# Optimization experiments

Hardware: AMD Instinct MI355X
Metric: run time of the kernel (lower is better)

## Reference

```python
import jax, jax.numpy as jnp
import numpy as np
from jax import lax

# config (mirrors Mamba3Config)
D_MODEL = 1024
D_STATE = 64
EXPAND = 2
HEADDIM = 64
D_INNER = EXPAND * D_MODEL            # 2048
NH = D_INNER // HEADDIM               # 32
N_ANG = D_STATE // 2                  # 32 rope angle channels
A_FLOOR = 1e-4
BATCH, SEQ = 2, 512
D_IN_PROJ = D_INNER + D_INNER + D_STATE + D_STATE + NH + NH + NH + N_ANG


def _layernorm(x, g, b, eps=1e-5):
    m = x.mean(-1, keepdims=True)
    v = ((x - m) ** 2).mean(-1, keepdims=True)
    return (x - m) / jnp.sqrt(v + eps) * g + b


def _rope_pairs(v, ang):
    # v: (..., S) even S; ang: (..., S//2). Rotate interleaved pairs.
    ve, vo = v[..., 0::2], v[..., 1::2]
    c, s = jnp.cos(ang), jnp.sin(ang)
    re = ve * c - vo * s
    ro = ve * s + vo * c
    return jnp.stack([re, ro], axis=-1).reshape(v.shape)


def setup_inputs() -> dict:
    key = jax.random.key(0)
    ks = jax.random.split(key, 9)
    u = jax.random.normal(ks[0], (BATCH, SEQ, D_MODEL), jnp.float32)
    W_in = jax.random.normal(ks[1], (D_MODEL, D_IN_PROJ), jnp.float32) * 0.02
    W_out = jax.random.normal(ks[2], (D_INNER, D_MODEL), jnp.float32) * 0.02
    dt_bias = jax.random.normal(ks[3], (NH,), jnp.float32) * 0.1
    D_param = jnp.ones((NH,), jnp.float32)
    Bn_g = 1.0 + 0.1 * jax.random.normal(ks[4], (D_STATE,), jnp.float32)
    Bn_b = 0.1 * jax.random.normal(ks[5], (D_STATE,), jnp.float32)
    Cn_g = 1.0 + 0.1 * jax.random.normal(ks[6], (D_STATE,), jnp.float32)
    Cn_b = 0.1 * jax.random.normal(ks[7], (D_STATE,), jnp.float32)
    return {"u": u, "W_in": W_in, "W_out": W_out, "dt_bias": dt_bias,
            "D_param": D_param, "Bn_g": Bn_g, "Bn_b": Bn_b,
            "Cn_g": Cn_g, "Cn_b": Cn_b}


def reference(u, W_in, W_out, dt_bias, D_param, Bn_g, Bn_b, Cn_g, Cn_b):
    B_, L, _ = u.shape
    proj = u @ W_in  # (B,L,D_IN_PROJ)
    idx = np.cumsum([D_INNER, D_INNER, D_STATE, D_STATE, NH, NH, NH])
    z, x, Bp, Cp, dd_dt, dd_A, trap_raw, angles = jnp.split(proj, idx, axis=-1)
    x4 = x.reshape(B_, L, NH, HEADDIM)
    z4 = z.reshape(B_, L, NH, HEADDIM)

    Bp = _layernorm(Bp, Bn_g, Bn_b)
    Cp = _layernorm(Cp, Cn_g, Cn_b)

    DT = jax.nn.softplus(dd_dt + dt_bias)            # (B,L,NH)
    DT_mean = DT.mean(axis=-1, keepdims=True)        # (B,L,1)
    phase = jnp.cumsum(angles * DT_mean, axis=1)     # (B,L,N_ANG)
    Bp_rot = _rope_pairs(Bp, phase)                  # (B,L,dS)
    Cp_rot = _rope_pairs(Cp, phase)

    A = jnp.minimum(-jax.nn.softplus(dd_A), -A_FLOOR)
    decay = jnp.exp(A * DT)                          # (B,L,NH)
    trap = jax.nn.sigmoid(trap_raw)                  # (B,L,NH)

    # Bx_all: (B,L,NH,hD,dS)  (B/C shared across heads -> broadcast in einsum)
    Bx = jnp.einsum('blhp,bln->blhpn', x4, Bp_rot)
    Bx_prev = jnp.pad(Bx[:, :-1], ((0, 0), (1, 0), (0, 0), (0, 0), (0, 0)))
    te = trap[..., None, None]
    inp = (te * Bx + (1.0 - te) * Bx_prev) * DT[..., None, None]

    # sequential selective scan over L
    decay_t = jnp.moveaxis(decay, 1, 0)   # (L,B,NH)
    inp_t = jnp.moveaxis(inp, 1, 0)       # (L,B,NH,hD,dS)
    C_t = jnp.moveaxis(Cp_rot, 1, 0)      # (L,B,dS)

    def step(h, xs):
        d, ip, c = xs
        h = d[:, :, None, None] * h + ip
        y = jnp.einsum('bhpn,bn->bhp', h, c)
        return h, y

    h0 = jnp.zeros((B_, NH, HEADDIM, D_STATE), u.dtype)
    _, ys = lax.scan(step, h0, (decay_t, inp_t, C_t))
    y = jnp.moveaxis(ys, 0, 1)                        # (B,L,NH,hD)
    y = (y + D_param[None, None, :, None] * x4) * jax.nn.silu(z4)
    out = y.reshape(B_, L, D_INNER) @ W_out
    return out
```

## Files before the change

### kernel.cpp

```cpp
#include <hip/hip_runtime.h>
#include <hip/hip_bf16.h>
#include <math.h>

#define B_   2
#define L_   512
#define DM   1024
#define DIP  4352
#define DPROJ 4224
#define DI   2048
#define NH_  32
#define HD   64
#define DS   64
#define NA   32
#define BL   (B_ * L_)
#define CHK  32
#define NCH  16
#define PB   (BL * 128)

#define OFF_Z    0
#define OFF_X    2048
#define OFF_BP   4096
#define OFF_CP   4160

typedef short bf16x8s __attribute__((ext_vector_type(8)));
typedef float f32x4 __attribute__((ext_vector_type(4)));

#define GL2LDS(gp, lp) __builtin_amdgcn_global_load_lds( \
    (const __attribute__((address_space(1))) unsigned int*)(const void*)(gp), \
    (__attribute__((address_space(3))) unsigned int*)(void*)(lp), 16, 0, 0)

__device__ __forceinline__ float softplusf(float x) {
    return x > 0.f ? x + log1pf(expf(-x)) : log1pf(expf(x));
}
__device__ __forceinline__ float sigmoidf_(float x) {
    return 1.f / (1.f + expf(-x));
}
__device__ __forceinline__ float wave_sum(float v) {
#pragma unroll
    for (int off = 32; off; off >>= 1) v += __shfl_xor(v, off);
    return v;
}
__device__ __forceinline__ ushort f2bf(float f) {
    uint u = __float_as_uint(f);
    return (ushort)((u + 0x7fffu + ((u >> 16) & 1u)) >> 16);
}
__device__ __forceinline__ float bf2f(ushort v) {
    return __uint_as_float((uint)v << 16);
}
__device__ __forceinline__ float4 ld_bf4(const ushort* p) {
    uint2 v = *(const uint2*)p;
    float4 r;
    r.x = __uint_as_float(v.x << 16);
    r.y = __uint_as_float(v.x & 0xffff0000u);
    r.z = __uint_as_float(v.y << 16);
    r.w = __uint_as_float(v.y & 0xffff0000u);
    return r;
}
__device__ __forceinline__ void st_bf4(ushort* p, float4 f) {
    uint2 v;
    v.x = (uint)f2bf(f.x) | ((uint)f2bf(f.y) << 16);
    v.y = (uint)f2bf(f.z) | ((uint)f2bf(f.w) << 16);
    *(uint2*)p = v;
}

__global__ __launch_bounds__(256) void prep_all(const float* __restrict__ u,
                                                const float* __restrict__ W_in,
                                                const float* __restrict__ W_out,
                                                ushort* __restrict__ ubf,
                                                ushort* __restrict__ WinT,
                                                ushort* __restrict__ WoutT,
                                                float* __restrict__ pbuf) {
    __shared__ float smem[2560];
    const int blk = blockIdx.x;
    const int tid = threadIdx.x;

    if (blk < 1600) {
        ushort (*t2)[72] = (ushort(*)[72])smem;
        const float* in;
        ushort* outp;
        int R, C, c0, r0;
        if (blk < 1088) {
            in = W_in; outp = WinT; R = DM; C = DIP;
            c0 = (blk % 68) * 64; r0 = (blk / 68) * 64;
        } else {
            const int bi = blk - 1088;
            in = W_out; outp = WoutT; R = DI; C = DM;
            c0 = (bi % 16) * 64; r0 = (bi / 16) * 64;
        }
        const int cq = tid & 15;
        const int rrb = tid >> 4;
#pragma unroll
        for (int j = 0; j < 4; ++j) {
            const int rr = j * 16 + rrb;
            float4 v = *(const float4*)&in[(size_t)(r0 + rr) * C + c0 + cq * 4];
            uint u0 = (uint)f2bf(v.x) | ((uint)f2bf(v.y) << 16);
            uint u1 = (uint)f2bf(v.z) | ((uint)f2bf(v.w) << 16);
            const int g = cq ^ ((rr >> 3) & 3);
            *(uint2*)&t2[rr][g * 4] = make_uint2(u0, u1);
        }
        __syncthreads();
        const int rq = tid & 7;
        const int ccb = tid >> 3;
#pragma unroll
        for (int j = 0; j < 2; ++j) {
            const int cc = j * 32 + ccb;
            ushort a[8];
#pragma unroll
            for (int i = 0; i < 8; ++i) {
                const int r = rq * 8 + i;
                const int g = (cc >> 2) ^ ((r >> 3) & 3);
                a[i] = t2[r][g * 4 + (cc & 3)];
            }
            uint4 w;
            w.x = (uint)a[0] | ((uint)a[1] << 16);
            w.y = (uint)a[2] | ((uint)a[3] << 16);
            w.z = (uint)a[4] | ((uint)a[5] << 16);
            w.w = (uint)a[6] | ((uint)a[7] << 16);
            *(uint4*)&outp[(size_t)(c0 + cc) * R + r0 + rq * 8] = w;
        }
        return;
    }
    if (blk < 2624) {
        const int i = (blk - 1600) * 256 + tid;
        float4 v = ((const float4*)u)[i];
        uint u0 = (uint)f2bf(v.x) | ((uint)f2bf(v.y) << 16);
        uint u1 = (uint)f2bf(v.z) | ((uint)f2bf(v.w) << 16);
        *(uint2*)&ubf[(size_t)i * 4] = make_uint2(u0, u1);
        return;
    }
    float (*us)[256] = (float(*)[256])smem;
    float* part = smem + 1024;
    const int sblk = blk - 2624;
    const int rb = sblk & 255;
    const int ks = sblk >> 8;
    const int blr = rb * 4;
    const int k0 = ks * 256;
    {
        const int r = tid >> 6, s = tid & 63;
        *(float4*)&us[r][s * 4] = *(const float4*)&u[(size_t)(blr + r) * DM + k0 + s * 4];
    }
    __syncthreads();
    const int col = tid & 127;
    const int half = tid >> 7;
    float s0 = 0.f, s1 = 0.f, s2 = 0.f, s3 = 0.f;
    const float* wp = W_in + (size_t)(k0 + half * 128) * DIP + 4224 + col;
#pragma unroll 16
    for (int k = 0; k < 128; ++k) {
        const float wv = wp[(size_t)k * DIP];
        s0 = fmaf(us[0][half * 128 + k], wv, s0);
        s1 = fmaf(us[1][half * 128 + k], wv, s1);
        s2 = fmaf(us[2][half * 128 + k], wv, s2);
        s3 = fmaf(us[3][half * 128 + k], wv, s3);
    }
    part[0 * 256 + tid] = s0; part[1 * 256 + tid] = s1;
    part[2 * 256 + tid] = s2; part[3 * 256 + tid] = s3;
    __syncthreads();
    if (tid < 128) {
#pragma unroll
        for (int r = 0; r < 4; ++r)
            pbuf[((size_t)ks * BL + blr + r) * 128 + tid] =
                part[r * 256 + tid] + part[r * 256 + 128 + tid];
    }
}

__global__ __launch_bounds__(256) void gemm_bf16(const ushort* __restrict__ A,
                                                 const ushort* __restrict__ BT,
                                                 float* __restrict__ C,
                                                 int K, int ldc, int kslice,
                                                 size_t partStride, int bf16out) {
    __shared__ ushort sA[2][64 * 64];
    __shared__ ushort sB[2][128 * 64];
    const int tid = threadIdx.x;
    const int l = tid & 63;
    const int wv = tid >> 6;
    const int wr = wv >> 1, wc = wv & 1;
    const int brow = blockIdx.y * 64;
    const int bcol = blockIdx.x * 128;
    const int kstart = blockIdx.z * kslice;
    float* Cp = C + (size_t)blockIdx.z * partStride;

    const int rr8 = l >> 3;
    const int swz = ((l & 7) ^ rr8) * 8;

    const ushort* gA0 = A + (size_t)(brow + wv * 16 + 0 + rr8) * K + kstart + swz;
    const ushort* gA1 = A + (size_t)(brow + wv * 16 + 8 + rr8) * K + kstart + swz;
    const ushort* gB0 = BT + (size_t)(bcol + wv * 32 + 0 + rr8) * K + kstart + swz;
    const ushort* gB1 = BT + (size_t)(bcol + wv * 32 + 8 + rr8) * K + kstart + swz;
    const ushort* gB2 = BT + (size_t)(bcol + wv * 32 + 16 + rr8) * K + kstart + swz;
    const ushort* gB3 = BT + (size_t)(bcol + wv * 32 + 24 + rr8) * K + kstart + swz;

    f32x4 acc[2][4] = {};

    GL2LDS(gA0, &sA[0][(wv * 16 + 0) * 64]);
    GL2LDS(gA1, &sA[0][(wv * 16 + 8) * 64]);
    GL2LDS(gB0, &sB[0][(wv * 32 + 0) * 64]);
    GL2LDS(gB1, &sB[0][(wv * 32 + 8) * 64]);
    GL2LDS(gB2, &sB[0][(wv * 32 + 16) * 64]);
    GL2LDS(gB3, &sB[0][(wv * 32 + 24) * 64]);
    __syncthreads();

    for (int k0 = 0; k0 < kslice; k0 += 64) {
        const int cur = (k0 >> 6) & 1;
        const int nxt = cur ^ 1;
        if (k0 + 64 < kslice) {
            GL2LDS(gA0 + k0 + 64, &sA[nxt][(wv * 16 + 0) * 64]);
            GL2LDS(gA1 + k0 + 64, &sA[nxt][(wv * 16 + 8) * 64]);
            GL2LDS(gB0 + k0 + 64, &sB[nxt][(wv * 32 + 0) * 64]);
            GL2LDS(gB1 + k0 + 64, &sB[nxt][(wv * 32 + 8) * 64]);
            GL2LDS(gB2 + k0 + 64, &sB[nxt][(wv * 32 + 16) * 64]);
            GL2LDS(gB3 + k0 + 64, &sB[nxt][(wv * 32 + 24) * 64]);
        }
        bf16x8s af[2][2], bfr[4][2];
#pragma unroll
        for (int m = 0; m < 2; ++m) {
            const int row = wr * 32 + m * 16 + (l & 15);
#pragma unroll
            for (int ks = 0; ks < 2; ++ks) {
                const int slot = (l >> 4) + ks * 4;
                af[m][ks] = *(const bf16x8s*)&sA[cur][(size_t)row * 64 + (slot ^ (row & 7)) * 8];
            }
        }
#pragma unroll
        for (int n = 0; n < 4; ++n) {
            const int row = wc * 64 + n * 16 + (l & 15);
#pragma unroll
            for (int ks = 0; ks < 2; ++ks) {
                const int slot = (l >> 4) + ks * 4;
                bfr[n][ks] = *(const bf16x8s*)&sB[cur][(size_t)row * 64 + (slot ^ (row & 7)) * 8];
            }
        }
#pragma unroll
        for (int ks = 0; ks < 2; ++ks)
#pragma unroll
            for (int m = 0; m < 2; ++m)
#pragma unroll
                for (int n = 0; n < 4; ++n)
                    acc[m][n] = __builtin_amdgcn_mfma_f32_16x16x32_bf16(af[m][ks], bfr[n][ks], acc[m][n], 0, 0, 0);
        __syncthreads();
    }
    if (bf16out) {
        ushort* Cb = (ushort*)Cp;
#pragma unroll
        for (int m = 0; m < 2; ++m) {
            const int row0 = brow + wr * 32 + m * 16 + (l >> 4) * 4;
#pragma unroll
            for (int n = 0; n < 4; ++n) {
                const int col = bcol + wc * 64 + n * 16 + (l & 15);
#pragma unroll
                for (int r = 0; r < 4; ++r)
                    Cb[(size_t)(row0 + r) * ldc + col] = f2bf(acc[m][n][r]);
            }
        }
    } else {
#pragma unroll
        for (int m = 0; m < 2; ++m) {
            const int row0 = brow + wr * 32 + m * 16 + (l >> 4) * 4;
#pragma unroll
            for (int n = 0; n < 4; ++n) {
                const int col = bcol + wc * 64 + n * 16 + (l & 15);
#pragma unroll
                for (int r = 0; r < 4; ++r)
                    Cp[(size_t)(row0 + r) * ldc + col] = acc[m][n][r];
            }
        }
    }
}

__global__ __launch_bounds__(256) void reduce4(const float* __restrict__ p,
                                               float* __restrict__ outp) {
    const int i = blockIdx.x * 256 + threadIdx.x;
    float4 a = ((const float4*)p)[i];
    float4 b = ((const float4*)(p + 1048576))[i];
    float4 c = ((const float4*)(p + 2097152))[i];
    float4 d = ((const float4*)(p + 3145728))[i];
    float4 s;
    s.x = (a.x + b.x) + (c.x + d.x);
    s.y = (a.y + b.y) + (c.y + d.y);
    s.z = (a.z + b.z) + (c.z + d.z);
    s.w = (a.w + b.w) + (c.w + d.w);
    ((float4*)outp)[i] = s;
}

__global__ __launch_bounds__(64) void small_ops(const ushort* __restrict__ projb,
                                                const float* __restrict__ pbuf,
                                                const float* __restrict__ dt_bias,
                                                const float* __restrict__ Bn_g,
                                                const float* __restrict__ Bn_b,
                                                const float* __restrict__ Cn_g,
                                                const float* __restrict__ Cn_b,
                                                float* __restrict__ DTa,
                                                float* __restrict__ deca,
                                                float* __restrict__ trpa,
                                                float* __restrict__ dtm,
                                                float* __restrict__ Bln,
                                                float* __restrict__ Cln) {
    const int bl = blockIdx.x;
    const int lane = threadIdx.x;
    const ushort* p = projb + (size_t)bl * DPROJ;

    float dt = 0.f;
    if (lane < NH_) {
        const size_t sb = (size_t)bl * 128 + lane;
        const float rdt = (pbuf[sb] + pbuf[PB + sb]) + (pbuf[2 * (size_t)PB + sb] + pbuf[3 * (size_t)PB + sb]);
        const float rda = (pbuf[sb + 32] + pbuf[PB + sb + 32]) + (pbuf[2 * (size_t)PB + sb + 32] + pbuf[3 * (size_t)PB + sb + 32]);
        const float rtr = (pbuf[sb + 64] + pbuf[PB + sb + 64]) + (pbuf[2 * (size_t)PB + sb + 64] + pbuf[3 * (size_t)PB + sb + 64]);
        dt = softplusf(rdt + dt_bias[lane]);
        DTa[bl * NH_ + lane] = dt;
        float a = -softplusf(rda);
        a = fminf(a, -1e-4f);
        deca[bl * NH_ + lane] = expf(a * dt);
        trpa[bl * NH_ + lane] = sigmoidf_(rtr);
    }
    float s = wave_sum(dt);
    if (lane == 0) dtm[bl] = s * (1.f / NH_);

    {
        float v = bf2f(p[OFF_BP + lane]);
        float m = wave_sum(v) * (1.f / 64.f);
        float d = v - m;
        float var = wave_sum(d * d) * (1.f / 64.f);
        Bln[bl * DS + lane] = d / sqrtf(var + 1e-5f) * Bn_g[lane] + Bn_b[lane];
    }
    {
        float v = bf2f(p[OFF_CP + lane]);
        float m = wave_sum(v) * (1.f / 64.f);
        float d = v - m;
        float var = wave_sum(d * d) * (1.f / 64.f);
        Cln[bl * DS + lane] = d / sqrtf(var + 1e-5f) * Cn_g[lane] + Cn_b[lane];
    }
}

__global__ __launch_bounds__(64) void phase_rope(const float* __restrict__ pbuf,
                                                 const float* __restrict__ dtm,
                                                 const float* __restrict__ Bln,
                                                 const float* __restrict__ Cln,
                                                 float* __restrict__ Brot,
                                                 float* __restrict__ Crot) {
    const int b = blockIdx.x >> 5;
    const int a = blockIdx.x & 31;
    const int lane = threadIdx.x;
    float s[8];
    float run = 0.f;
#pragma unroll
    for (int j = 0; j < 8; ++j) {
        const int bl = b * L_ + lane * 8 + j;
        const size_t sb = (size_t)bl * 128 + 96 + a;
        const float ang = (pbuf[sb] + pbuf[PB + sb]) +
                          (pbuf[2 * (size_t)PB + sb] + pbuf[3 * (size_t)PB + sb]);
        run += ang * dtm[bl];
        s[j] = run;
    }
    float inc = run;
#pragma unroll
    for (int off = 1; off < 64; off <<= 1) {
        float v = __shfl_up(inc, off);
        if (lane >= off) inc += v;
    }
    const float excl = inc - run;
#pragma unroll
    for (int j = 0; j < 8; ++j) {
        const int bl = b * L_ + lane * 8 + j;
        const float ph = excl + s[j];
        float sn, cs;
        __sincosf(ph, &sn, &cs);
        {
            float ve = Bln[bl * DS + 2 * a], vo = Bln[bl * DS + 2 * a + 1];
            Brot[bl * DS + 2 * a]     = ve * cs - vo * sn;
            Brot[bl * DS + 2 * a + 1] = ve * sn + vo * cs;
        }
        {
            float ve = Cln[bl * DS + 2 * a], vo = Cln[bl * DS + 2 * a + 1];
            Crot[bl * DS + 2 * a]     = ve * cs - vo * sn;
            Crot[bl * DS + 2 * a + 1] = ve * sn + vo * cs;
        }
    }
}

__global__ __launch_bounds__(512, 8) void scanA(const ushort* __restrict__ projb,
                                                const float* __restrict__ Brot,
                                                const float* __restrict__ Crot,
                                                const float* __restrict__ DTa,
                                                const float* __restrict__ deca,
                                                const float* __restrict__ trpa,
                                                ushort* __restrict__ yactb,
                                                ushort* __restrict__ hendb) {
    __shared__ float Ball[CHK + 1][64];
    __shared__ float Call[CHK][64];
    __shared__ float Xall[CHK + 1][64];
    __shared__ float sa_[CHK], sb_[CHK], sdl[CHK];
    __shared__ float ypart[8][4][64];
    const int blk = blockIdx.x;
    const int c  = blk & 15;
    const int bh = blk >> 4;
    const int h  = bh & 31;
    const int b  = bh >> 5;
    const int tid = threadIdx.x;
    const int lane = tid & 63;
    const int wv = tid >> 6;
    const int bl0 = b * L_ + c * CHK;

    if (wv == 0) {
        Ball[0][lane] = (c > 0) ? Brot[(bl0 - 1) * DS + lane] : 0.f;
        Xall[0][lane] = (c > 0) ? bf2f(projb[(size_t)(bl0 - 1) * DPROJ + OFF_X + h * HD + lane]) : 0.f;
    }
    for (int r = wv; r < CHK; r += 8) {
        Ball[r + 1][lane] = Brot[(bl0 + r) * DS + lane];
        Call[r][lane]     = Crot[(bl0 + r) * DS + lane];
        Xall[r + 1][lane] = bf2f(projb[(size_t)(bl0 + r) * DPROJ + OFF_X + h * HD + lane]);
    }
    if (tid < CHK) {
        float d  = deca[(bl0 + tid) * NH_ + h];
        float dt = DTa[(bl0 + tid) * NH_ + h];
        float te = trpa[(bl0 + tid) * NH_ + h];
        sdl[tid] = d;
        sa_[tid] = dt * te;
        sb_[tid] = dt * (1.f - te);
    }
    __syncthreads();

    float4 h4[2], bp[2];
#pragma unroll
    for (int q = 0; q < 2; ++q) {
        h4[q] = make_float4(0.f, 0.f, 0.f, 0.f);
        bp[q] = *(const float4*)&Ball[0][(wv * 2 + q) * 4];
    }
    float xp = Xall[0][lane];

#pragma unroll
    for (int qt = 0; qt < 8; ++qt) {
#pragma unroll
        for (int i8 = 0; i8 < 4; ++i8) {
            const int i = qt * 4 + i8;
            const float xi = Xall[i + 1][lane];
            const float ac = sa_[i] * xi;
            const float bc = sb_[i] * xp;
            const float d  = sdl[i];
            float yi = 0.f;
#pragma unroll
            for (int q = 0; q < 2; ++q) {
                const float4 bb = *(const float4*)&Ball[i + 1][(wv * 2 + q) * 4];
                const float4 cc = *(const float4*)&Call[i][(wv * 2 + q) * 4];
                h4[q].x = fmaf(d, h4[q].x, fmaf(ac, bb.x, bc * bp[q].x));
                h4[q].y = fmaf(d, h4[q].y, fmaf(ac, bb.y, bc * bp[q].y));
                h4[q].z = fmaf(d, h4[q].z, fmaf(ac, bb.z, bc * bp[q].z));
                h4[q].w = fmaf(d, h4[q].w, fmaf(ac, bb.w, bc * bp[q].w));
                yi = fmaf(h4[q].x, cc.x, yi);
                yi = fmaf(h4[q].y, cc.y, yi);
                yi = fmaf(h4[q].z, cc.z, yi);
                yi = fmaf(h4[q].w, cc.w, yi);
                bp[q] = bb;
            }
            xp = xi;
            ypart[wv][i8][lane] = yi;
        }
        __syncthreads();
        if (wv < 4) {
            const int il = wv;
            const float s = ((ypart[0][il][lane] + ypart[1][il][lane]) +
                             (ypart[2][il][lane] + ypart[3][il][lane])) +
                            ((ypart[4][il][lane] + ypart[5][il][lane]) +
                             (ypart[6][il][lane] + ypart[7][il][lane]));
            yactb[(size_t)(bl0 + qt * 4 + il) * DI + h * HD + lane] = f2bf(s);
        }
        __syncthreads();
    }
    const size_t hbase = (size_t)(bh * NCH + c) * 4096;
#pragma unroll
    for (int q = 0; q < 2; ++q) {
        const int n4 = wv * 2 + q;
        const size_t hb = hbase + (size_t)(n4 * 4) * 64 + lane;
        hendb[hb]       = f2bf(h4[q].x);
        hendb[hb + 64]  = f2bf(h4[q].y);
        hendb[hb + 128] = f2bf(h4[q].z);
        hendb[hb + 192] = f2bf(h4[q].w);
    }
}

__global__ __launch_bounds__(256) void scanB(const float* __restrict__ deca,
                                             ushort* __restrict__ hendb) {
    __shared__ float Pl[NCH];
    const int bh = blockIdx.x >> 2;
    const int slice = blockIdx.x & 3;
    const int h = bh & 31, b = bh >> 5;
    const int tid = threadIdx.x;
    if (tid < NCH) {
        float p = 1.f;
        for (int j = 0; j < CHK; ++j)
            p *= deca[(b * L_ + tid * CHK + j) * NH_ + h];
        Pl[tid] = p;
    }
    __syncthreads();
    const size_t eoff = (size_t)slice * 1024 + tid * 4;
    const size_t cbase = (size_t)bh * NCH * 4096;
    float4 run = make_float4(0.f, 0.f, 0.f, 0.f);
    float4 cur = ld_bf4(&hendb[cbase + eoff]);
    float4 nx  = ld_bf4(&hendb[cbase + 4096 + eoff]);
    for (int cc = 0; cc < NCH - 1; ++cc) {
        float4 fut = make_float4(0.f, 0.f, 0.f, 0.f);
        if (cc + 2 <= NCH - 2)
            fut = ld_bf4(&hendb[cbase + (size_t)(cc + 2) * 4096 + eoff]);
        const float Pc = Pl[cc];
        run.x = fmaf(Pc, run.x, cur.x);
        run.y = fmaf(Pc, run.y, cur.y);
        run.z = fmaf(Pc, run.z, cur.z);
        run.w = fmaf(Pc, run.w, cur.w);
        st_bf4(&hendb[cbase + (size_t)cc * 4096 + eoff], run);
        cur = nx; nx = fut;
    }
}

__global__ __launch_bounds__(256) void scanC(const ushort* __restrict__ projb,
                                             const float* __restrict__ Crot,
                                             const float* __restrict__ deca,
                                             const ushort* __restrict__ hendb,
                                             const float* __restrict__ D_param,
                                             const ushort* __restrict__ yactb,
                                             ushort* __restrict__ ybf) {
    __shared__ float Call[CHK][64];
    __shared__ float sdl[CHK];
    __shared__ float wcum[CHK];
    __shared__ float cpart[4][16][64];
    const int blk = blockIdx.x;
    const int c = blk & 15;
    const int bh = blk >> 4;
    const int h = bh & 31, b = bh >> 5;
    const int tid = threadIdx.x;
    const int lane = tid & 63;
    const int wv = tid >> 6;
    const int bl0 = b * L_ + c * CHK;

    for (int r = wv; r < CHK; r += 4)
        Call[r][lane] = Crot[(bl0 + r) * DS + lane];
    if (tid < CHK) sdl[tid] = deca[(bl0 + tid) * NH_ + h];

    float4 h0[4];
    if (c > 0) {
        const size_t base = (size_t)(bh * NCH + (c - 1)) * 4096;
#pragma unroll
        for (int q = 0; q < 4; ++q) {
            const int n4 = wv * 4 + q;
            h0[q].x = bf2f(hendb[base + (size_t)(n4 * 4 + 0) * 64 + lane]);
            h0[q].y = bf2f(hendb[base + (size_t)(n4 * 4 + 1) * 64 + lane]);
            h0[q].z = bf2f(hendb[base + (size_t)(n4 * 4 + 2) * 64 + lane]);
            h0[q].w = bf2f(hendb[base + (size_t)(n4 * 4 + 3) * 64 + lane]);
        }
    } else {
#pragma unroll
        for (int q = 0; q < 4; ++q) h0[q] = make_float4(0.f, 0.f, 0.f, 0.f);
    }
    __syncthreads();
    if (tid < CHK) {
        float p = 1.f;
        for (int k = 0; k <= tid; ++k) p *= sdl[k];
        wcum[tid] = p;
    }

    const float Dp = D_param[h];
#pragma unroll
    for (int half = 0; half < 2; ++half) {
#pragma unroll
        for (int i16 = 0; i16 < 16; ++i16) {
            const int i = half * 16 + i16;
            float s = 0.f;
#pragma unroll
            for (int q = 0; q < 4; ++q) {
                const float4 cc = *(const float4*)&Call[i][(wv * 4 + q) * 4];
                s = fmaf(h0[q].x, cc.x, s);
                s = fmaf(h0[q].y, cc.y, s);
                s = fmaf(h0[q].z, cc.z, s);
                s = fmaf(h0[q].w, cc.w, s);
            }
            cpart[wv][i16][lane] = s;
        }
        __syncthreads();
#pragma unroll
        for (int k = 0; k < 4; ++k) {
            const int il = wv * 4 + k;
            const int i  = half * 16 + il;
            const int bl = bl0 + i;
            const float s = (cpart[0][il][lane] + cpart[1][il][lane]) +
                            (cpart[2][il][lane] + cpart[3][il][lane]);
            const float xv = bf2f(projb[(size_t)bl * DPROJ + OFF_X + h * HD + lane]);
            const float zv = bf2f(projb[(size_t)bl * DPROJ + OFF_Z + h * HD + lane]);
            const float ya = bf2f(yactb[(size_t)bl * DI + h * HD + lane]);
            const float yv = ya + wcum[i] * s + Dp * xv;
            ybf[(size_t)bl * DI + h * HD + lane] = f2bf(yv * zv * sigmoidf_(zv));
        }
        __syncthreads();
    }
}

extern "C" void kernel_launch(void* const* d_in, const int* in_sizes, int n_in,
                              void* d_out, int out_size, void* d_ws, size_t ws_size,
                              hipStream_t stream) {
    const float* u       = (const float*)d_in[0];
    const float* W_in    = (const float*)d_in[1];
    const float* W_out   = (const float*)d_in[2];
    const float* dt_bias = (const float*)d_in[3];
    const float* D_param = (const float*)d_in[4];
    const float* Bn_g    = (const float*)d_in[5];
    const float* Bn_b    = (const float*)d_in[6];
    const float* Cn_g    = (const float*)d_in[7];
    const float* Cn_b    = (const float*)d_in[8];
    float* out = (float*)d_out;

    float* ws    = (float*)d_ws;
    float* proj  = ws;
    float* Bln   = proj + (size_t)BL * DIP;
    float* Cln   = Bln + BL * DS;
    float* Brot  = Cln + BL * DS;
    float* Crot  = Brot + BL * DS;
    float* DTa   = Crot + BL * DS;
    float* deca  = DTa + BL * NH_;
    float* trpa  = deca + BL * NH_;
    float* dtm   = trpa + BL * NH_;
    float* phase = dtm + BL;
    float* yact  = phase + BL * NA;
    float* ybf_f = yact + (size_t)BL * DI;
    float* wout_f= ybf_f + (size_t)BL * DI / 2;
    float* shreg = wout_f + (size_t)DM * DI / 2;
    float* pbuf  = shreg + 4194304;

    ushort* projb = (ushort*)proj;
    ushort* ubf   = (ushort*)yact;
    ushort* yactb = (ushort*)yact;
    ushort* WinT  = (ushort*)shreg;
    ushort* hendb = (ushort*)shreg;
    float*  cpart = shreg;
    ushort* WoutT = (ushort*)wout_f;
    ushort* ybf   = (ushort*)ybf_f;

    prep_all<<<dim3(1600 + 1024 + 1024), dim3(256), 0, stream>>>(
        u, W_in, W_out, ubf, WinT, WoutT, pbuf);
    gemm_bf16<<<dim3(33, 16, 1), dim3(256), 0, stream>>>(ubf, WinT, proj, DM, DPROJ, DM,
                                                         0, 1);
    small_ops<<<dim3(BL), dim3(64), 0, stream>>>(projb, pbuf, dt_bias, Bn_g, Bn_b, Cn_g, Cn_b,
                                                 DTa, deca, trpa, dtm, Bln, Cln);
    phase_rope<<<dim3(B_ * NA), dim3(64), 0, stream>>>(pbuf, dtm, Bln, Cln, Brot, Crot);
    scanA<<<dim3(B_ * NH_ * NCH), dim3(512), 0, stream>>>(projb, Brot, Crot, DTa, deca, trpa,
                                                          yactb, hendb);
    scanB<<<dim3(B_ * NH_ * 4), dim3(256), 0, stream>>>(deca, hendb);
    scanC<<<dim3(B_ * NH_ * NCH), dim3(256), 0, stream>>>(projb, Crot, deca, hendb, D_param,
                                                          yactb, ybf);
    gemm_bf16<<<dim3(8, 16, 4), dim3(256), 0, stream>>>(ybf, WoutT, cpart, DI, DM, DI / 4,
                                                        (size_t)BL * DM, 0);
    reduce4<<<dim3(1024), dim3(256), 0, stream>>>(cpart, out);
}
```

Measured before the change: 106.1 us.

## Remap scanA threads to head-dim rows with shuffle reduction and bf16 B/C staging

Changes the intra-chunk scan's thread mapping so each 8-lane group owns one head-dim row and splits the 64 state columns into 8 per lane. The y reduction becomes three warp shuffles in place of an LDS partial-sum buffer, which removes the two block-wide barriers per 4 timesteps. B and C are staged in shared memory as bf16 and unpacked with bit shifts, halving LDS footprint and read traffic. The cost is lower B/C precision in the state update and a scattered, uncoalesced yact write done by only one lane in eight.

```diff
diff --git a/kernel.cpp b/kernel.cpp
--- a/kernel.cpp
+++ b/kernel.cpp
@@ -376,19 +376,18 @@
     }
 }
 
-__global__ __launch_bounds__(512, 8) void scanA(const ushort* __restrict__ projb,
-                                                const float* __restrict__ Brot,
-                                                const float* __restrict__ Crot,
-                                                const float* __restrict__ DTa,
-                                                const float* __restrict__ deca,
-                                                const float* __restrict__ trpa,
-                                                ushort* __restrict__ yactb,
-                                                ushort* __restrict__ hendb) {
-    __shared__ float Ball[CHK + 1][64];
-    __shared__ float Call[CHK][64];
-    __shared__ float Xall[CHK + 1][64];
-    __shared__ float sa_[CHK], sb_[CHK], sdl[CHK];
-    __shared__ float ypart[8][4][64];
+__global__ __launch_bounds__(512) void scanA(const ushort* __restrict__ projb,
+                                             const float* __restrict__ Brot,
+                                             const float* __restrict__ Crot,
+                                             const float* __restrict__ DTa,
+                                             const float* __restrict__ deca,
+                                             const float* __restrict__ trpa,
+                                             ushort* __restrict__ yactb,
+                                             ushort* __restrict__ hendb) {
+    __shared__ ushort Bb[CHK + 1][64];
+    __shared__ ushort Cb[CHK][64];
+    __shared__ float  Xall[CHK + 1][64];
+    __shared__ float  sa_[CHK], sb_[CHK], sdl[CHK];
     const int blk = blockIdx.x;
     const int c  = blk & 15;
     const int bh = blk >> 4;
@@ -397,15 +396,18 @@
     const int tid = threadIdx.x;
     const int lane = tid & 63;
     const int wv = tid >> 6;
+    const int pi = lane >> 3;
+    const int ng = lane & 7;
+    const int p  = wv * 8 + pi;
     const int bl0 = b * L_ + c * CHK;
 
     if (wv == 0) {
-        Ball[0][lane] = (c > 0) ? Brot[(bl0 - 1) * DS + lane] : 0.f;
+        Bb[0][lane]   = (c > 0) ? f2bf(Brot[(bl0 - 1) * DS + lane]) : (ushort)0;
         Xall[0][lane] = (c > 0) ? bf2f(projb[(size_t)(bl0 - 1) * DPROJ + OFF_X + h * HD + lane]) : 0.f;
     }
     for (int r = wv; r < CHK; r += 8) {
-        Ball[r + 1][lane] = Brot[(bl0 + r) * DS + lane];
-        Call[r][lane]     = Crot[(bl0 + r) * DS + lane];
+        Bb[r + 1][lane] = f2bf(Brot[(bl0 + r) * DS + lane]);
+        Cb[r][lane]     = f2bf(Crot[(bl0 + r) * DS + lane]);
         Xall[r + 1][lane] = bf2f(projb[(size_t)(bl0 + r) * DPROJ + OFF_X + h * HD + lane]);
     }
     if (tid < CHK) {
@@ -418,62 +420,53 @@
     }
     __syncthreads();
 
-    float4 h4[2], bp[2];
-#pragma unroll
-    for (int q = 0; q < 2; ++q) {
-        h4[q] = make_float4(0.f, 0.f, 0.f, 0.f);
-        bp[q] = *(const float4*)&Ball[0][(wv * 2 + q) * 4];
-    }
-    float xp = Xall[0][lane];
-
-#pragma unroll
-    for (int qt = 0; qt < 8; ++qt) {
-#pragma unroll
-        for (int i8 = 0; i8 < 4; ++i8) {
-            const int i = qt * 4 + i8;
-            const float xi = Xall[i + 1][lane];
-            const float ac = sa_[i] * xi;
-            const float bc = sb_[i] * xp;
-            const float d  = sdl[i];
-            float yi = 0.f;
-#pragma unroll
-            for (int q = 0; q < 2; ++q) {
-                const float4 bb = *(const float4*)&Ball[i + 1][(wv * 2 + q) * 4];
-                const float4 cc = *(const float4*)&Call[i][(wv * 2 + q) * 4];
-                h4[q].x = fmaf(d, h4[q].x, fmaf(ac, bb.x, bc * bp[q].x));
-                h4[q].y = fmaf(d, h4[q].y, fmaf(ac, bb.y, bc * bp[q].y));
-                h4[q].z = fmaf(d, h4[q].z, fmaf(ac, bb.z, bc * bp[q].z));
-                h4[q].w = fmaf(d, h4[q].w, fmaf(ac, bb.w, bc * bp[q].w));
-                yi = fmaf(h4[q].x, cc.x, yi);
-                yi = fmaf(h4[q].y, cc.y, yi);
-                yi = fmaf(h4[q].z, cc.z, yi);
-                yi = fmaf(h4[q].w, cc.w, yi);
-                bp[q] = bb;
-            }
-            xp = xi;
-            ypart[wv][i8][lane] = yi;
-        }
-        __syncthreads();
-        if (wv < 4) {
-            const int il = wv;
-            const float s = ((ypart[0][il][lane] + ypart[1][il][lane]) +
-                             (ypart[2][il][lane] + ypart[3][il][lane])) +
-                            ((ypart[4][il][lane] + ypart[5][il][lane]) +
-                             (ypart[6][il][lane] + ypart[7][il][lane]));
-            yactb[(size_t)(bl0 + qt * 4 + il) * DI + h * HD + lane] = f2bf(s);
-        }
-        __syncthreads();
+    float hreg[8], bp[8];
+#pragma unroll
+    for (int j = 0; j < 8; ++j) hreg[j] = 0.f;
+    {
+        uint4 w = *(const uint4*)&Bb[0][ng * 8];
+        bp[0] = __uint_as_float(w.x << 16);  bp[1] = __uint_as_float(w.x & 0xffff0000u);
+        bp[2] = __uint_as_float(w.y << 16);  bp[3] = __uint_as_float(w.y & 0xffff0000u);
+        bp[4] = __uint_as_float(w.z << 16);  bp[5] = __uint_as_float(w.z & 0xffff0000u);
+        bp[6] = __uint_as_float(w.w << 16);  bp[7] = __uint_as_float(w.w & 0xffff0000u);
+    }
+    float xp = Xall[0][p];
+
+#pragma unroll 4
+    for (int i = 0; i < CHK; ++i) {
+        const float xi = Xall[i + 1][p];
+        const float ac = sa_[i] * xi;
+        const float bc = sb_[i] * xp;
+        const float d  = sdl[i];
+        const uint4 wb = *(const uint4*)&Bb[i + 1][ng * 8];
+        const uint4 wc = *(const uint4*)&Cb[i][ng * 8];
+        float bb[8], cc[8];
+        bb[0] = __uint_as_float(wb.x << 16);  bb[1] = __uint_as_float(wb.x & 0xffff0000u);
+        bb[2] = __uint_as_float(wb.y << 16);  bb[3] = __uint_as_float(wb.y & 0xffff0000u);
+        bb[4] = __uint_as_float(wb.z << 16);  bb[5] = __uint_as_float(wb.z & 0xffff0000u);
+        bb[6] = __uint_as_float(wb.w << 16);  bb[7] = __uint_as_float(wb.w & 0xffff0000u);
+        cc[0] = __uint_as_float(wc.x << 16);  cc[1] = __uint_as_float(wc.x & 0xffff0000u);
+        cc[2] = __uint_as_float(wc.y << 16);  cc[3] = __uint_as_float(wc.y & 0xffff0000u);
+        cc[4] = __uint_as_float(wc.z << 16);  cc[5] = __uint_as_float(wc.z & 0xffff0000u);
+        cc[6] = __uint_as_float(wc.w << 16);  cc[7] = __uint_as_float(wc.w & 0xffff0000u);
+        float yi = 0.f;
+#pragma unroll
+        for (int j = 0; j < 8; ++j) {
+            hreg[j] = fmaf(d, hreg[j], fmaf(ac, bb[j], bc * bp[j]));
+            yi = fmaf(hreg[j], cc[j], yi);
+            bp[j] = bb[j];
+        }
+        xp = xi;
+        yi += __shfl_xor(yi, 1);
+        yi += __shfl_xor(yi, 2);
+        yi += __shfl_xor(yi, 4);
+        if (ng == 0)
+            yactb[(size_t)(bl0 + i) * DI + h * HD + p] = f2bf(yi);
     }
     const size_t hbase = (size_t)(bh * NCH + c) * 4096;
 #pragma unroll
-    for (int q = 0; q < 2; ++q) {
-        const int n4 = wv * 2 + q;
-        const size_t hb = hbase + (size_t)(n4 * 4) * 64 + lane;
-        hendb[hb]       = f2bf(h4[q].x);
-        hendb[hb + 64]  = f2bf(h4[q].y);
-        hendb[hb + 128] = f2bf(h4[q].z);
-        hendb[hb + 192] = f2bf(h4[q].w);
-    }
+    for (int j = 0; j < 8; ++j)
+        hendb[hbase + (size_t)(ng * 8 + j) * 64 + p] = f2bf(hreg[j]);
 }
 
 __global__ __launch_bounds__(256) void scanB(const float* __restrict__ deca,
```

Result: slower. 112.8 us (+6.4%).
